# Optimization experiments

Measured on AMD Instinct MI355X. Metric: run time of the kernel, lower is better.

The kernel has to match this reference:

```python
import jax, jax.numpy as jnp
import numpy as np

EMBED_DIM = 4096
POLY_PTS = 32
POLY_DIM = POLY_PTS * 2  # 64
LN_EPS = 1e-5


def setup_inputs() -> dict:
    key = jax.random.key(0)
    ks = jax.random.split(key, 12)
    B, N, Dmax = 8, 1024, POLY_DIM
    s = 0.02
    return {
        "prompts": jax.random.normal(ks[0], (B, N, Dmax), dtype=jnp.float32),
        "prompt_types": jax.random.randint(ks[1], (B, N), 0, 3, dtype=jnp.int64),
        # point encoder: Linear(2, E)
        "point_w": jax.random.normal(ks[2], (EMBED_DIM, 2), dtype=jnp.float32) * s,
        "point_b": jax.random.normal(ks[3], (EMBED_DIM,), dtype=jnp.float32) * s,
        # box encoder: Linear(4, E)
        "box_w": jax.random.normal(ks[4], (EMBED_DIM, 4), dtype=jnp.float32) * s,
        "box_b": jax.random.normal(ks[5], (EMBED_DIM,), dtype=jnp.float32) * s,
        # polygon encoder: Linear(64,E) -> LayerNorm(E) -> ReLU -> Linear(E,E)
        "poly_w1": jax.random.normal(ks[6], (EMBED_DIM, POLY_DIM), dtype=jnp.float32) * s,
        "poly_b1": jax.random.normal(ks[7], (EMBED_DIM,), dtype=jnp.float32) * s,
        "ln_gamma": jnp.ones((EMBED_DIM,), dtype=jnp.float32),
        "ln_beta": jnp.zeros((EMBED_DIM,), dtype=jnp.float32),
        "poly_w2": jax.random.normal(ks[8], (EMBED_DIM, EMBED_DIM), dtype=jnp.float32) * s,
        "poly_b2": jax.random.normal(ks[9], (EMBED_DIM,), dtype=jnp.float32) * s,
        # type embedding table (3, E)
        "type_emb": jax.random.normal(ks[10], (3, EMBED_DIM), dtype=jnp.float32) * s,
    }


def _layernorm(x, gamma, beta):
    mu = jnp.mean(x, axis=-1, keepdims=True)
    var = jnp.mean(jnp.square(x - mu), axis=-1, keepdims=True)
    return (x - mu) * jax.lax.rsqrt(var + LN_EPS) * gamma + beta


def reference(prompts, prompt_types, point_w, point_b, box_w, box_b,
              poly_w1, poly_b1, ln_gamma, ln_beta, poly_w2, poly_b2, type_emb):
    # Per-type expert encodings computed densely, then selected by type mask
    # (same math as torch's masked gather -> linear -> scatter).
    pt = jnp.einsum('bnd,ed->bne', prompts[..., :2], point_w) + point_b + type_emb[0]
    bx = jnp.einsum('bnd,ed->bne', prompts[..., :4], box_w) + box_b + type_emb[1]
    h = jnp.einsum('bnd,ed->bne', prompts[..., :POLY_DIM], poly_w1) + poly_b1
    h = jax.nn.relu(_layernorm(h, ln_gamma, ln_beta))
    pg = jnp.einsum('bnd,ed->bne', h, poly_w2) + poly_b2 + type_emb[2]
    t = prompt_types[..., None]
    zeros = jnp.zeros_like(pt)
    out = jnp.where(t == 0, pt, zeros) + jnp.where(t == 1, bx, zeros) + jnp.where(t == 2, pg, zeros)
    return out
```

## Files before the change

kernel.cpp:

```cpp
#include <hip/hip_runtime.h>

#define EMBED 4096
#define NTOK 8192
#define LN_EPS 1e-5f

#define NB_CONVW2 (EMBED * EMBED / (256 * 8))
#define NB_CONVW1 (EMBED * 64 / (256 * 8))

typedef float f4_t __attribute__((ext_vector_type(4)));
typedef __bf16 bf16x8 __attribute__((ext_vector_type(8)));
typedef unsigned short us8_t __attribute__((ext_vector_type(8)));

__device__ __forceinline__ unsigned short f2bf(float f) {
    unsigned int u = __float_as_uint(f);
    u += 0x7fffu + ((u >> 16) & 1u);
    return (unsigned short)(u >> 16);
}

typedef const __attribute__((address_space(1))) unsigned int gas_t;
typedef __attribute__((address_space(3))) unsigned int las_t;

__device__ __forceinline__ void gl_lds16(const void* g, void* l) {
    __builtin_amdgcn_global_load_lds((gas_t*)g, (las_t*)l, 16, 0, 0);
}

__device__ __forceinline__ void conv_body(const float* __restrict__ src,
                                          unsigned short* __restrict__ dst,
                                          int i) {
    const f4_t* in4 = (const f4_t*)src;
    f4_t v0 = in4[(size_t)i * 2];
    f4_t v1 = in4[(size_t)i * 2 + 1];
    us8_t o;
    o[0] = f2bf(v0.x); o[1] = f2bf(v0.y); o[2] = f2bf(v0.z); o[3] = f2bf(v0.w);
    o[4] = f2bf(v1.x); o[5] = f2bf(v1.y); o[6] = f2bf(v1.z); o[7] = f2bf(v1.w);
    *(us8_t*)(dst + (size_t)i * 8) = o;
}

__global__ __launch_bounds__(256) void k_prep(
    const float* __restrict__ prompts, const int* __restrict__ types,
    const float* __restrict__ pw, const float* __restrict__ pb,
    const float* __restrict__ bw, const float* __restrict__ bb,
    const float* __restrict__ temb,
    const float* __restrict__ w1, const float* __restrict__ b1,
    const float* __restrict__ w2,
    int* __restrict__ idx, int* __restrict__ counters,
    float* __restrict__ G, float* __restrict__ cbar,
    unsigned short* __restrict__ w1b, unsigned short* __restrict__ w2b,
    float* __restrict__ out)
{
    int bid = blockIdx.x;
    int t = threadIdx.x;

    if (bid == 0) {
        __shared__ int cnt;
        if (t == 0) cnt = 0;
        __syncthreads();
        for (int i = t; i < NTOK; i += 256) {
            if (types[i] == 2) {
                int s = atomicAdd(&cnt, 1);
                idx[s] = i;
            }
        }
        __syncthreads();
        if (t == 0) {
            counters[0] = cnt;
            counters[1] = (cnt + 127) & ~127;
        }
        return;
    }

    if (bid <= 66) {
        int i = bid - 1;
        int wave = t >> 6, lane = t & 63;
        float part[17];
#pragma unroll
        for (int jj = 0; jj < 17; ++jj) part[jj] = 0.f;
        for (int e = lane; e < EMBED; e += 64) {
            const f4_t* row4 = (const f4_t*)(w1 + (size_t)e * 64);
            float be = b1[e];
            float ai = (i < 64) ? w1[(size_t)e * 64 + i] : ((i == 64) ? be : 1.f);
            f4_t r0 = row4[wave * 4 + 0];
            f4_t r1 = row4[wave * 4 + 1];
            f4_t r2 = row4[wave * 4 + 2];
            f4_t r3 = row4[wave * 4 + 3];
            part[0]  += ai * r0.x; part[1]  += ai * r0.y;
            part[2]  += ai * r0.z; part[3]  += ai * r0.w;
            part[4]  += ai * r1.x; part[5]  += ai * r1.y;
            part[6]  += ai * r1.z; part[7]  += ai * r1.w;
            part[8]  += ai * r2.x; part[9]  += ai * r2.y;
            part[10] += ai * r2.z; part[11] += ai * r2.w;
            part[12] += ai * r3.x; part[13] += ai * r3.y;
            part[14] += ai * r3.z; part[15] += ai * r3.w;
            if (wave == 3) part[16] += ai * be;
        }
#pragma unroll
        for (int jj = 0; jj < 17; ++jj) {
            float v = part[jj];
            v += __shfl_down(v, 32);
            v += __shfl_down(v, 16);
            v += __shfl_down(v, 8);
            v += __shfl_down(v, 4);
            v += __shfl_down(v, 2);
            v += __shfl_down(v, 1);
            part[jj] = v;
        }
        if (lane == 0) {
            int nj = (wave == 3) ? 17 : 16;
            for (int jj = 0; jj < nj; ++jj) {
                int j = (jj == 16) ? 64 : (wave * 16 + jj);
                float s = part[jj] * (1.f / 4096.f);
                if (i < 65) G[i * 65 + j] = s;
                else        cbar[j] = s;
            }
        }
        return;
    }

    if (bid < 67 + NB_CONVW2) {
        conv_body(w2, w2b, (bid - 67) * 256 + t);
        return;
    }

    if (bid < 67 + NB_CONVW2 + NB_CONVW1) {
        conv_body(w1, w1b, (bid - 67 - NB_CONVW2) * 256 + t);
        return;
    }

    {
        int token = bid - (67 + NB_CONVW2 + NB_CONVW1);
        int ty = types[token];
        if (ty >= 2) return;
        const float* x = prompts + (size_t)token * 64;
        float x0 = x[0], x1 = x[1], x2 = x[2], x3 = x[3];
        f4_t* o4 = (f4_t*)(out + (size_t)token * EMBED);
        if (ty == 0) {
            const f4_t* w4 = (const f4_t*)pw;
            const f4_t* b4 = (const f4_t*)pb;
            const f4_t* te4 = (const f4_t*)temb;
#pragma unroll
            for (int j = 0; j < 4; ++j) {
                int e4 = t + 256 * j;
                f4_t wa = w4[e4 * 2], wb = w4[e4 * 2 + 1];
                f4_t bv = b4[e4], tv = te4[e4];
                f4_t r;
                r.x = x0 * wa.x + x1 * wa.y + bv.x + tv.x;
                r.y = x0 * wa.z + x1 * wa.w + bv.y + tv.y;
                r.z = x0 * wb.x + x1 * wb.y + bv.z + tv.z;
                r.w = x0 * wb.z + x1 * wb.w + bv.w + tv.w;
                o4[e4] = r;
            }
        } else {
            const f4_t* w4 = (const f4_t*)bw;
            const f4_t* b4 = (const f4_t*)bb;
            const f4_t* te4 = (const f4_t*)(temb + EMBED);
#pragma unroll
            for (int j = 0; j < 4; ++j) {
                int e4 = t + 256 * j;
                f4_t w0 = w4[e4 * 4 + 0], w1v = w4[e4 * 4 + 1];
                f4_t w2v = w4[e4 * 4 + 2], w3v = w4[e4 * 4 + 3];
                f4_t bv = b4[e4], tv = te4[e4];
                f4_t r;
                r.x = x0 * w0.x + x1 * w0.y + x2 * w0.z + x3 * w0.w + bv.x + tv.x;
                r.y = x0 * w1v.x + x1 * w1v.y + x2 * w1v.z + x3 * w1v.w + bv.y + tv.y;
                r.z = x0 * w2v.x + x1 * w2v.y + x2 * w2v.z + x3 * w2v.w + bv.z + tv.z;
                r.w = x0 * w3v.x + x1 * w3v.y + x2 * w3v.z + x3 * w3v.w + bv.w + tv.w;
                o4[e4] = r;
            }
        }
    }
}

__global__ __launch_bounds__(256) void k_stats(const float* __restrict__ prompts,
                                               const int* __restrict__ idx,
                                               const int* __restrict__ counters,
                                               const float* __restrict__ cbar,
                                               const float* __restrict__ G,
                                               float* __restrict__ mu,
                                               float* __restrict__ rstd,
                                               unsigned short* __restrict__ xbuf) {
    int count = counters[0], padded = counters[1];
    int base = blockIdx.x * 4;
    if (base >= padded) return;
    __shared__ float sG[65 * 65];
    __shared__ __align__(16) float xs[4][66];
    int t = threadIdx.x;
    for (int v = t; v < 65 * 65; v += 256) sG[v] = G[v];
    int r = t >> 6, lane = t & 63;
    int m = base + r;
    bool vld = (m < count);
    float xv = vld ? prompts[(size_t)idx[m] * 64 + lane] : 0.f;
    xs[r][lane] = xv;
    if (lane == 0) xs[r][64] = vld ? 1.f : 0.f;
    xbuf[(size_t)m * 64 + lane] = vld ? f2bf(xv) : (unsigned short)0;
    __syncthreads();
    float mu_p, m2_p;
    {
        float xi = xs[r][lane];
        mu_p = cbar[lane] * xi;
        const float* Gr = sG + lane * 65;
        float rd = 0.f;
        for (int j = 0; j < 65; ++j) rd += Gr[j] * xs[r][j];
        m2_p = xi * rd;
    }
    if (lane == 0) {
        float xi = xs[r][64];
        mu_p += cbar[64] * xi;
        const float* Gr = sG + 64 * 65;
        float rd = 0.f;
        for (int j = 0; j < 65; ++j) rd += Gr[j] * xs[r][j];
        m2_p += xi * rd;
    }
    for (int off = 32; off > 0; off >>= 1) {
        mu_p += __shfl_down(mu_p, off);
        m2_p += __shfl_down(m2_p, off);
    }
    if (lane == 0) {
        if (vld) {
            mu[m] = mu_p;
            rstd[m] = rsqrtf(fmaxf(m2_p - mu_p * mu_p, 0.f) + LN_EPS);
        } else {
            mu[m] = 0.f;
            rstd[m] = 0.f;
        }
    }
}

__global__ __launch_bounds__(256) void k_lin1m(const unsigned short* __restrict__ xbuf,
                                               const unsigned short* __restrict__ w1b,
                                               const int* __restrict__ counters,
                                               const float* __restrict__ b1,
                                               const float* __restrict__ gamma,
                                               const float* __restrict__ beta,
                                               const float* __restrict__ mu,
                                               const float* __restrict__ rstd,
                                               unsigned short* __restrict__ hbuf) {
    int padded = counters[1];
    int m0 = blockIdx.y * 128;
    if (m0 >= padded) return;
    int n0 = blockIdx.x * 128;

    __shared__ unsigned short At[2][128 * 32];
    __shared__ unsigned short Bt[2][128 * 32];

    int t = threadIdx.x;
    int lane = t & 63, wave = t >> 6;
    int wm = (wave >> 1) * 64;
    int wn = (wave & 1) * 64;

    int srow = t >> 2, skg = t & 3;
    const unsigned short* Ag = xbuf + (size_t)(m0 + srow) * 64 + skg * 8;
    const unsigned short* Bg = w1b + (size_t)(n0 + srow) * 64 + skg * 8;
    char* A0 = (char*)At[0]; char* A1 = (char*)At[1];
    char* B0 = (char*)Bt[0]; char* B1 = (char*)Bt[1];
    int ldsw = (t & ~63) * 16;

    f4_t acc[4][4];
#pragma unroll
    for (int i = 0; i < 4; ++i)
#pragma unroll
        for (int j = 0; j < 4; ++j) acc[i][j] = (f4_t)0.f;

    int fr = lane & 15;
    int quad = lane >> 4;

    gl_lds16(Ag,                A0 + ldsw);
    gl_lds16(Ag + 64 * 64,      A0 + 4096 + ldsw);
    gl_lds16(Ag + 32,           A1 + ldsw);
    gl_lds16(Ag + 64 * 64 + 32, A1 + 4096 + ldsw);
    gl_lds16(Bg,                B0 + ldsw);
    gl_lds16(Bg + 64 * 64,      B0 + 4096 + ldsw);
    gl_lds16(Bg + 32,           B1 + ldsw);
    gl_lds16(Bg + 64 * 64 + 32, B1 + 4096 + ldsw);
    __syncthreads();

    {
        bf16x8 a[4], b[4];
#pragma unroll
        for (int i = 0; i < 4; ++i) {
            a[i] = *(const bf16x8*)(A0 + (wm + i * 16 + fr) * 64 + quad * 16);
            b[i] = *(const bf16x8*)(B0 + (wn + i * 16 + fr) * 64 + quad * 16);
        }
#pragma unroll
        for (int i = 0; i < 4; ++i)
#pragma unroll
            for (int j = 0; j < 4; ++j)
                acc[i][j] = __builtin_amdgcn_mfma_f32_16x16x32_bf16(a[i], b[j], acc[i][j], 0, 0, 0);
#pragma unroll
        for (int i = 0; i < 4; ++i) {
            a[i] = *(const bf16x8*)(A1 + (wm + i * 16 + fr) * 64 + quad * 16);
            b[i] = *(const bf16x8*)(B1 + (wn + i * 16 + fr) * 64 + quad * 16);
        }
#pragma unroll
        for (int i = 0; i < 4; ++i)
#pragma unroll
            for (int j = 0; j < 4; ++j)
                acc[i][j] = __builtin_amdgcn_mfma_f32_16x16x32_bf16(a[i], b[j], acc[i][j], 0, 0, 0);
    }

#pragma unroll
    for (int i = 0; i < 4; ++i) {
#pragma unroll
        for (int r = 0; r < 4; ++r) {
            int grow = m0 + wm + i * 16 + quad * 4 + r;
            float muv = mu[grow], rsv = rstd[grow];
            unsigned short* hrow = hbuf + (size_t)grow * EMBED;
#pragma unroll
            for (int j = 0; j < 4; ++j) {
                int gcol = n0 + wn + j * 16 + fr;
                float h = (acc[i][j][r] + b1[gcol] - muv) * rsv * gamma[gcol] + beta[gcol];
                hrow[gcol] = f2bf(fmaxf(h, 0.f));
            }
        }
    }
}

__global__ __launch_bounds__(256) void k_gemm(const unsigned short* __restrict__ hbuf,
                                              const unsigned short* __restrict__ w2b,
                                              const int* __restrict__ idx,
                                              const int* __restrict__ counters,
                                              const float* __restrict__ b2,
                                              const float* __restrict__ te2,
                                              float* __restrict__ out) {
    int count = counters[0], padded = counters[1];
    int m0 = blockIdx.y * 128;
    if (m0 >= padded) return;
    int n0 = blockIdx.x * 128;

    __shared__ unsigned short At[2][128 * 32];
    __shared__ unsigned short Bt[2][128 * 32];

    int t = threadIdx.x;
    int lane = t & 63, wave = t >> 6;
    int wm = (wave >> 1) * 64;
    int wn = (wave & 1) * 64;

    int srow = t >> 2, skg = t & 3;
    const unsigned short* Ag = hbuf + (size_t)(m0 + srow) * EMBED + skg * 8;
    const unsigned short* Bg = w2b + (size_t)(n0 + srow) * EMBED + skg * 8;
    char* A0 = (char*)At[0]; char* A1 = (char*)At[1];
    char* B0 = (char*)Bt[0]; char* B1 = (char*)Bt[1];
    int ldsw = (t & ~63) * 16;

    f4_t acc[4][4];
#pragma unroll
    for (int i = 0; i < 4; ++i)
#pragma unroll
        for (int j = 0; j < 4; ++j) acc[i][j] = (f4_t)0.f;

    int fr = lane & 15;
    int quad = lane >> 4;

    for (int k0 = 0; k0 < EMBED; k0 += 64) {
        __syncthreads();
        gl_lds16(Ag + k0,                   A0 + ldsw);
        gl_lds16(Ag + 64 * EMBED + k0,      A0 + 4096 + ldsw);
        gl_lds16(Ag + k0 + 32,              A1 + ldsw);
        gl_lds16(Ag + 64 * EMBED + k0 + 32, A1 + 4096 + ldsw);
        gl_lds16(Bg + k0,                   B0 + ldsw);
        gl_lds16(Bg + 64 * EMBED + k0,      B0 + 4096 + ldsw);
        gl_lds16(Bg + k0 + 32,              B1 + ldsw);
        gl_lds16(Bg + 64 * EMBED + k0 + 32, B1 + 4096 + ldsw);
        __syncthreads();

        bf16x8 a[4], b[4];
#pragma unroll
        for (int i = 0; i < 4; ++i) {
            a[i] = *(const bf16x8*)(A0 + (wm + i * 16 + fr) * 64 + quad * 16);
            b[i] = *(const bf16x8*)(B0 + (wn + i * 16 + fr) * 64 + quad * 16);
        }
#pragma unroll
        for (int i = 0; i < 4; ++i)
#pragma unroll
            for (int j = 0; j < 4; ++j)
                acc[i][j] = __builtin_amdgcn_mfma_f32_16x16x32_bf16(a[i], b[j], acc[i][j], 0, 0, 0);
#pragma unroll
        for (int i = 0; i < 4; ++i) {
            a[i] = *(const bf16x8*)(A1 + (wm + i * 16 + fr) * 64 + quad * 16);
            b[i] = *(const bf16x8*)(B1 + (wn + i * 16 + fr) * 64 + quad * 16);
        }
#pragma unroll
        for (int i = 0; i < 4; ++i)
#pragma unroll
            for (int j = 0; j < 4; ++j)
                acc[i][j] = __builtin_amdgcn_mfma_f32_16x16x32_bf16(a[i], b[j], acc[i][j], 0, 0, 0);
    }

#pragma unroll
    for (int i = 0; i < 4; ++i) {
#pragma unroll
        for (int r = 0; r < 4; ++r) {
            int grow = m0 + wm + i * 16 + quad * 4 + r;
            if (grow < count) {
                float* orow = out + (size_t)idx[grow] * EMBED;
#pragma unroll
                for (int j = 0; j < 4; ++j) {
                    int gcol = n0 + wn + j * 16 + fr;
                    orow[gcol] = acc[i][j][r] + b2[gcol] + te2[gcol];
                }
            }
        }
    }
}

extern "C" void kernel_launch(void* const* d_in, const int* in_sizes, int n_in,
                              void* d_out, int out_size, void* d_ws, size_t ws_size,
                              hipStream_t stream) {
    const float* prompts  = (const float*)d_in[0];
    const int*   types    = (const int*)d_in[1];
    const float* point_w  = (const float*)d_in[2];
    const float* point_b  = (const float*)d_in[3];
    const float* box_w    = (const float*)d_in[4];
    const float* box_b    = (const float*)d_in[5];
    const float* poly_w1  = (const float*)d_in[6];
    const float* poly_b1  = (const float*)d_in[7];
    const float* ln_g     = (const float*)d_in[8];
    const float* ln_b     = (const float*)d_in[9];
    const float* poly_w2  = (const float*)d_in[10];
    const float* poly_b2  = (const float*)d_in[11];
    const float* type_emb = (const float*)d_in[12];
    float* out = (float*)d_out;

    char* ws = (char*)d_ws;
    int*   counters = (int*)ws;
    int*   idx      = (int*)(ws + 256);
    float* cbar     = (float*)(ws + 33280);
    float* G        = (float*)(ws + 33792);
    float* muarr    = (float*)(ws + 51200);
    float* rstdarr  = (float*)(ws + 84224);
    unsigned short* xbuf = (unsigned short*)(ws + 131072);
    unsigned short* w1b  = (unsigned short*)(ws + 131072 + 1048576);
    unsigned short* w2b  = (unsigned short*)(ws + 2097152);
    unsigned short* hbuf = (unsigned short*)(ws + 2097152 + (size_t)EMBED * EMBED * 2);

    int nprep = 67 + NB_CONVW2 + NB_CONVW1 + NTOK;
    k_prep<<<nprep, 256, 0, stream>>>(prompts, types, point_w, point_b,
                                      box_w, box_b, type_emb,
                                      poly_w1, poly_b1, poly_w2,
                                      idx, counters, G, cbar, w1b, w2b, out);
    k_stats<<<NTOK / 4, 256, 0, stream>>>(prompts, idx, counters, cbar, G,
                                          muarr, rstdarr, xbuf);
    k_lin1m<<<dim3(EMBED / 128, NTOK / 128), 256, 0, stream>>>(
        xbuf, w1b, counters, poly_b1, ln_g, ln_b, muarr, rstdarr, hbuf);
    k_gemm<<<dim3(EMBED / 128, NTOK / 128), 256, 0, stream>>>(
        hbuf, w2b, idx, counters, poly_b2, type_emb + 2 * EMBED, out);
}
```

Before: 404.5 us.

## Stage W1 rows in LDS for Gram kernel and halve GEMM K-tile

The Gram-matrix blocks now load 64-row chunks of W1 and b1 into shared memory with coalesced vector loads, then read each lane's row from LDS instead of issuing strided per-lane global loads. Both MFMA GEMM kernels drop from a 64-wide K step held in two LDS buffers to a 32-wide K step in a single buffer. The LDS footprint is halved, which could allow more resident blocks, but the number of loop iterations and barrier pairs doubles. The LDS tile layout looks questionable: the loads write 16 bytes per thread at a 64-byte row stride, yet rows are read back at a 64-byte stride as well, so correctness depends on the unseen layout assumptions.

Result: faster. 382.5 us (-5.4%).

```diff
diff --git a/kernel.cpp b/kernel.cpp
--- a/kernel.cpp
+++ b/kernel.cpp
@@ -71,27 +71,30 @@
 
     if (bid <= 66) {
         int i = bid - 1;
+        __shared__ float sA[64][66];
         int wave = t >> 6, lane = t & 63;
         float part[17];
 #pragma unroll
         for (int jj = 0; jj < 17; ++jj) part[jj] = 0.f;
-        for (int e = lane; e < EMBED; e += 64) {
-            const f4_t* row4 = (const f4_t*)(w1 + (size_t)e * 64);
-            float be = b1[e];
-            float ai = (i < 64) ? w1[(size_t)e * 64 + i] : ((i == 64) ? be : 1.f);
-            f4_t r0 = row4[wave * 4 + 0];
-            f4_t r1 = row4[wave * 4 + 1];
-            f4_t r2 = row4[wave * 4 + 2];
-            f4_t r3 = row4[wave * 4 + 3];
-            part[0]  += ai * r0.x; part[1]  += ai * r0.y;
-            part[2]  += ai * r0.z; part[3]  += ai * r0.w;
-            part[4]  += ai * r1.x; part[5]  += ai * r1.y;
-            part[6]  += ai * r1.z; part[7]  += ai * r1.w;
-            part[8]  += ai * r2.x; part[9]  += ai * r2.y;
-            part[10] += ai * r2.z; part[11] += ai * r2.w;
-            part[12] += ai * r3.x; part[13] += ai * r3.y;
-            part[14] += ai * r3.z; part[15] += ai * r3.w;
-            if (wave == 3) part[16] += ai * be;
+        for (int e0 = 0; e0 < EMBED; e0 += 64) {
+            __syncthreads();
+#pragma unroll
+            for (int q = 0; q < 4; ++q) {
+                int v = t + 256 * q;
+                int r = v >> 4, c4 = v & 15;
+                f4_t val = *(const f4_t*)(w1 + (size_t)(e0 + r) * 64 + c4 * 4);
+                sA[r][c4 * 4 + 0] = val.x;
+                sA[r][c4 * 4 + 1] = val.y;
+                sA[r][c4 * 4 + 2] = val.z;
+                sA[r][c4 * 4 + 3] = val.w;
+            }
+            if (t < 64) sA[t][64] = b1[e0 + t];
+            __syncthreads();
+            float ai = (i < 65) ? sA[lane][i] : 1.f;
+#pragma unroll
+            for (int jj = 0; jj < 16; ++jj)
+                part[jj] += ai * sA[lane][wave * 16 + jj];
+            if (wave == 3) part[16] += ai * sA[lane][64];
         }
 #pragma unroll
         for (int jj = 0; jj < 17; ++jj) {
@@ -239,8 +242,8 @@
     if (m0 >= padded) return;
     int n0 = blockIdx.x * 128;
 
-    __shared__ unsigned short At[2][128 * 32];
-    __shared__ unsigned short Bt[2][128 * 32];
+    __shared__ unsigned short At[128 * 32];
+    __shared__ unsigned short Bt[128 * 32];
 
     int t = threadIdx.x;
     int lane = t & 63, wave = t >> 6;
@@ -250,8 +253,8 @@
     int srow = t >> 2, skg = t & 3;
     const unsigned short* Ag = xbuf + (size_t)(m0 + srow) * 64 + skg * 8;
     const unsigned short* Bg = w1b + (size_t)(n0 + srow) * 64 + skg * 8;
-    char* A0 = (char*)At[0]; char* A1 = (char*)At[1];
-    char* B0 = (char*)Bt[0]; char* B1 = (char*)Bt[1];
+    char* AtC = (char*)At;
+    char* BtC = (char*)Bt;
     int ldsw = (t & ~63) * 16;
 
     f4_t acc[4][4];
@@ -263,32 +266,20 @@
     int fr = lane & 15;
     int quad = lane >> 4;
 
-    gl_lds16(Ag,                A0 + ldsw);
-    gl_lds16(Ag + 64 * 64,      A0 + 4096 + ldsw);
-    gl_lds16(Ag + 32,           A1 + ldsw);
-    gl_lds16(Ag + 64 * 64 + 32, A1 + 4096 + ldsw);
-    gl_lds16(Bg,                B0 + ldsw);
-    gl_lds16(Bg + 64 * 64,      B0 + 4096 + ldsw);
-    gl_lds16(Bg + 32,           B1 + ldsw);
-    gl_lds16(Bg + 64 * 64 + 32, B1 + 4096 + ldsw);
-    __syncthreads();
-
-    {
+#pragma unroll
+    for (int k0 = 0; k0 < 64; k0 += 32) {
+        __syncthreads();
+        gl_lds16(Ag + k0,            AtC + ldsw);
+        gl_lds16(Ag + 64 * 64 + k0,  AtC + 4096 + ldsw);
+        gl_lds16(Bg + k0,            BtC + ldsw);
+        gl_lds16(Bg + 64 * 64 + k0,  BtC + 4096 + ldsw);
+        __syncthreads();
+
         bf16x8 a[4], b[4];
 #pragma unroll
         for (int i = 0; i < 4; ++i) {
-            a[i] = *(const bf16x8*)(A0 + (wm + i * 16 + fr) * 64 + quad * 16);
-            b[i] = *(const bf16x8*)(B0 + (wn + i * 16 + fr) * 64 + quad * 16);
-        }
-#pragma unroll
-        for (int i = 0; i < 4; ++i)
-#pragma unroll
-            for (int j = 0; j < 4; ++j)
-                acc[i][j] = __builtin_amdgcn_mfma_f32_16x16x32_bf16(a[i], b[j], acc[i][j], 0, 0, 0);
-#pragma unroll
-        for (int i = 0; i < 4; ++i) {
-            a[i] = *(const bf16x8*)(A1 + (wm + i * 16 + fr) * 64 + quad * 16);
-            b[i] = *(const bf16x8*)(B1 + (wn + i * 16 + fr) * 64 + quad * 16);
+            a[i] = *(const bf16x8*)(AtC + (wm + i * 16 + fr) * 64 + quad * 16);
+            b[i] = *(const bf16x8*)(BtC + (wn + i * 16 + fr) * 64 + quad * 16);
         }
 #pragma unroll
         for (int i = 0; i < 4; ++i)
@@ -326,8 +317,8 @@
     if (m0 >= padded) return;
     int n0 = blockIdx.x * 128;
 
-    __shared__ unsigned short At[2][128 * 32];
-    __shared__ unsigned short Bt[2][128 * 32];
+    __shared__ unsigned short At[128 * 32];
+    __shared__ unsigned short Bt[128 * 32];
 
     int t = threadIdx.x;
     int lane = t & 63, wave = t >> 6;
@@ -337,8 +328,8 @@
     int srow = t >> 2, skg = t & 3;
     const unsigned short* Ag = hbuf + (size_t)(m0 + srow) * EMBED + skg * 8;
     const unsigned short* Bg = w2b + (size_t)(n0 + srow) * EMBED + skg * 8;
-    char* A0 = (char*)At[0]; char* A1 = (char*)At[1];
-    char* B0 = (char*)Bt[0]; char* B1 = (char*)Bt[1];
+    char* AtC = (char*)At;
+    char* BtC = (char*)Bt;
     int ldsw = (t & ~63) * 16;
 
     f4_t acc[4][4];
@@ -350,33 +341,19 @@
     int fr = lane & 15;
     int quad = lane >> 4;
 
-    for (int k0 = 0; k0 < EMBED; k0 += 64) {
-        __syncthreads();
-        gl_lds16(Ag + k0,                   A0 + ldsw);
-        gl_lds16(Ag + 64 * EMBED + k0,      A0 + 4096 + ldsw);
-        gl_lds16(Ag + k0 + 32,              A1 + ldsw);
-        gl_lds16(Ag + 64 * EMBED + k0 + 32, A1 + 4096 + ldsw);
-        gl_lds16(Bg + k0,                   B0 + ldsw);
-        gl_lds16(Bg + 64 * EMBED + k0,      B0 + 4096 + ldsw);
-        gl_lds16(Bg + k0 + 32,              B1 + ldsw);
-        gl_lds16(Bg + 64 * EMBED + k0 + 32, B1 + 4096 + ldsw);
+    for (int k0 = 0; k0 < EMBED; k0 += 32) {
+        __syncthreads();
+        gl_lds16(Ag + k0,               AtC + ldsw);
+        gl_lds16(Ag + 64 * EMBED + k0,  AtC + 4096 + ldsw);
+        gl_lds16(Bg + k0,               BtC + ldsw);
+        gl_lds16(Bg + 64 * EMBED + k0,  BtC + 4096 + ldsw);
         __syncthreads();
 
         bf16x8 a[4], b[4];
 #pragma unroll
         for (int i = 0; i < 4; ++i) {
-            a[i] = *(const bf16x8*)(A0 + (wm + i * 16 + fr) * 64 + quad * 16);
-            b[i] = *(const bf16x8*)(B0 + (wn + i * 16 + fr) * 64 + quad * 16);
-        }
-#pragma unroll
-        for (int i = 0; i < 4; ++i)
-#pragma unroll
-            for (int j = 0; j < 4; ++j)
-                acc[i][j] = __builtin_amdgcn_mfma_f32_16x16x32_bf16(a[i], b[j], acc[i][j], 0, 0, 0);
-#pragma unroll
-        for (int i = 0; i < 4; ++i) {
-            a[i] = *(const bf16x8*)(A1 + (wm + i * 16 + fr) * 64 + quad * 16);
-            b[i] = *(const bf16x8*)(B1 + (wn + i * 16 + fr) * 64 + quad * 16);
+            a[i] = *(const bf16x8*)(AtC + (wm + i * 16 + fr) * 64 + quad * 16);
+            b[i] = *(const bf16x8*)(BtC + (wn + i * 16 + fr) * 64 + quad * 16);
         }
 #pragma unroll
         for (int i = 0; i < 4; ++i)
```
